# Performance work log

Hardware: AMD Instinct MI355X
Metric: run time of the kernel (lower is better)

## Reference

```python
import jax, jax.numpy as jnp
import numpy as np

B, D, C, OUT = 16384, 784, 2048, 10

def setup_inputs() -> dict:
    key = jax.random.key(0)
    k1, k2, k3 = jax.random.split(key, 3)
    x = jax.random.normal(k1, (B, D), dtype=jnp.float32)
    centres = jax.random.normal(k2, (C, D), dtype=jnp.float32)
    log_sigmas = jnp.zeros((C,), dtype=jnp.float32)
    W = jax.random.normal(k3, (OUT, C), dtype=jnp.float32) * (1.0 / np.sqrt(C))
    b = jnp.zeros((OUT,), dtype=jnp.float32)
    return {"x": x, "centres": centres, "log_sigmas": log_sigmas, "W": W, "b": b}

def reference(x, centres, log_sigmas, W, b):
    # (B, C, D) broadcast tensor the torch code materializes; same math).
    x2 = jnp.sum(x * x, axis=-1, keepdims=True)          # (B, 1)
    c2 = jnp.sum(centres * centres, axis=-1)             # (C,)
    d2 = jnp.maximum(x2 + c2[None, :] - 2.0 * (x @ centres.T), 0.0)  # (B, C)
    distances = jnp.sqrt(d2) / jnp.exp(log_sigmas)[None, :]          # (B, C)
    phi = jnp.exp(-(distances * distances))              # gaussian basis
    return phi @ W.T + b                                  # (B, OUT)
```

## Files before the change

kernel.cpp:

```cpp
#include <hip/hip_runtime.h>


#define B_ROWS 16384
#define D_DIM  784
#define C_DIM  2048
#define NOUT   10
#define KPAD   832
#define NKC    26
#define NCG    128
#define LOG2E  1.4426950408889634f

typedef __attribute__((ext_vector_type(8))) __bf16 bf16x8;
typedef __attribute__((ext_vector_type(4))) float  f32x4;
typedef __attribute__((ext_vector_type(4))) unsigned short ushort4v;

__device__ __forceinline__ unsigned short f2bf(float f) {
  union { float f; unsigned int u; } v; v.f = f;
  unsigned int u = v.u;
  return (unsigned short)((u + 0x7fffu + ((u >> 16) & 1u)) >> 16);
}

__device__ __forceinline__ void async16(const __bf16* g, __bf16* l) {
  __builtin_amdgcn_global_load_lds((const __attribute__((address_space(1))) void*)g,
                                   (__attribute__((address_space(3))) void*)l,
                                   16, 0, 0);
}

__global__ __launch_bounds__(256) void prep_rows(const float* __restrict__ src,
                                                 unsigned short* __restrict__ dst,
                                                 float* __restrict__ sq) {
  const int row  = blockIdx.x * 4 + (threadIdx.x >> 6);
  const int lane = threadIdx.x & 63;
  const float* s = src + (size_t)row * D_DIM;
  unsigned short* d = dst + (size_t)row * KPAD;
  float acc = 0.f;
#pragma unroll
  for (int c = 0; c < 4; ++c) {
    const int ch = lane + c * 64;
    if (ch < 196) {
      const float4 v = ((const float4*)s)[ch];
      ushort4v o; o.x = f2bf(v.x); o.y = f2bf(v.y); o.z = f2bf(v.z); o.w = f2bf(v.w);
      *(ushort4v*)(d + ch * 4) = o;
      acc += v.x * v.x + v.y * v.y + v.z * v.z + v.w * v.w;
    } else if (ch < 208) {
      ushort4v z = {0, 0, 0, 0};
      *(ushort4v*)(d + ch * 4) = z;
    }
  }
#pragma unroll
  for (int off = 32; off > 0; off >>= 1) acc += __shfl_down(acc, off);
  if (lane == 0) sq[row] = acc;
}

__global__ __launch_bounds__(256) void prep_cpack(const float* __restrict__ cen,
                                                  unsigned short* __restrict__ dst) {
  const int tile = blockIdx.x * 4 + (threadIdx.x >> 6);
  const int lane = threadIdx.x & 63;
  const int kc = tile >> 7;
  const int cg = tile & 127;
  const int c  = cg * 16 + (lane & 15);
  const int k  = kc * 32 + (lane >> 4) * 8;
  ushort4v o0 = {0, 0, 0, 0}, o1 = {0, 0, 0, 0};
  if (k + 8 <= D_DIM) {
    const float4 v0 = *(const float4*)(cen + (size_t)c * D_DIM + k);
    const float4 v1 = *(const float4*)(cen + (size_t)c * D_DIM + k + 4);
    o0.x = f2bf(v0.x); o0.y = f2bf(v0.y); o0.z = f2bf(v0.z); o0.w = f2bf(v0.w);
    o1.x = f2bf(v1.x); o1.y = f2bf(v1.y); o1.z = f2bf(v1.z); o1.w = f2bf(v1.w);
  }
  unsigned short* p = dst + ((size_t)tile * 64 + lane) * 8;
  *(ushort4v*)p = o0;
  *(ushort4v*)(p + 4) = o1;
}

__global__ __launch_bounds__(256) void prep_csq(const float* __restrict__ cen,
                                                float* __restrict__ sq) {
  const int row  = blockIdx.x * 4 + (threadIdx.x >> 6);
  const int lane = threadIdx.x & 63;
  const float* s = cen + (size_t)row * D_DIM;
  float acc = 0.f;
#pragma unroll
  for (int c = 0; c < 4; ++c) {
    const int ch = lane + c * 64;
    if (ch < 196) {
      const float4 v = ((const float4*)s)[ch];
      acc += v.x * v.x + v.y * v.y + v.z * v.z + v.w * v.w;
    }
  }
#pragma unroll
  for (int off = 32; off > 0; off >>= 1) acc += __shfl_down(acc, off);
  if (lane == 0) sq[row] = acc;
}

__global__ __launch_bounds__(256) void prep_misc(const float* __restrict__ ls,
                                                 const float* __restrict__ W,
                                                 const float* __restrict__ bias,
                                                 float* __restrict__ scale,
                                                 unsigned short* __restrict__ wb,
                                                 float* __restrict__ out) {
  const int i = blockIdx.x * 256 + threadIdx.x;
  if (i < B_ROWS * NOUT) out[i] = bias[i % NOUT];
  const int j = i - B_ROWS * NOUT;
  if (j >= 0 && j < 16 * C_DIM)
    wb[j] = ((j >> 11) < NOUT) ? f2bf(W[(j >> 11) * C_DIM + (j & 2047)]) : (unsigned short)0;
  const int k = j - 16 * C_DIM;
  if (k >= 0 && k < C_DIM) scale[k] = __expf(-2.f * ls[k]) * LOG2E;
}

__global__ __launch_bounds__(256, 4) void rbf_main(
    const __bf16* __restrict__ xb, const bf16x8* __restrict__ cbp,
    const __bf16* __restrict__ wb,
    const float* __restrict__ x2, const float* __restrict__ c2,
    const float* __restrict__ scale, float* __restrict__ out) {
  __shared__ char smem[34816];
  __bf16* As = (__bf16*)smem;
  __bf16* Ph = (__bf16*)smem;
  __shared__ float x2s[128], c2s[128], scs[128];

  const int tid  = threadIdx.x;
  const int w    = tid >> 6;
  const int lane = tid & 63;
  const int q    = lane >> 4;
  const int l16  = lane & 15;
  const int brow = blockIdx.x * 128;
  const int bcol = blockIdx.y * 128;

  if (tid < 128) x2s[tid] = x2[brow + tid];
  else { c2s[tid - 128] = c2[bcol + tid - 128]; scs[tid - 128] = scale[bcol + tid - 128]; }

  const int srow = tid >> 3;
  const int skc  = (tid & 7) ^ (srow & 7);
  const __bf16* gA = xb + (size_t)(brow + srow) * KPAD + skc * 8;
  __bf16* lA = As + w * 512;

  const int wr = (w >> 1) * 64;
  const int wc = (w & 1) * 64;
  const int cgb = (bcol >> 4) + (w & 1) * 4;
  const int swz = l16 & 7;

  f32x4 acc[4][4] = {};

#pragma unroll 1
  for (int it = 0; it < NKC / 2; ++it) {
    const int k0 = it * 64;
#pragma unroll
    for (int r = 0; r < 4; ++r)
      async16(gA + (size_t)r * 32 * KPAD + k0, lA + r * 2048);
    __syncthreads();
#pragma unroll
    for (int ks = 0; ks < 2; ++ks) {
      const int kc = it * 2 + ks;
      bf16x8 af[4], bfr[4];
#pragma unroll
      for (int j = 0; j < 4; ++j)
        bfr[j] = cbp[((size_t)kc * NCG + cgb + j) * 64 + lane];
#pragma unroll
      for (int i = 0; i < 4; ++i)
        af[i] = *(const bf16x8*)&As[(wr + i * 16 + l16) * 64 + (((ks * 4 + q) ^ swz) << 3)];
#pragma unroll
      for (int i = 0; i < 4; ++i)
#pragma unroll
        for (int j = 0; j < 4; ++j)
          acc[i][j] = __builtin_amdgcn_mfma_f32_16x16x32_bf16(af[i], bfr[j], acc[i][j], 0, 0, 0);
    }
    __syncthreads();
  }

#pragma unroll
  for (int i = 0; i < 4; ++i) {
    float xv[4];
#pragma unroll
    for (int r = 0; r < 4; ++r) xv[r] = x2s[wr + i * 16 + q * 4 + r];
#pragma unroll
    for (int j = 0; j < 4; ++j) {
      const int cl = wc + j * 16 + l16;
      const float c2v = c2s[cl];
      const float sc = scs[cl];
#pragma unroll
      for (int r = 0; r < 4; ++r) {
        const int rl = wr + i * 16 + q * 4 + r;
        const float d2 = fmaxf(fmaf(-2.f, acc[i][j][r], xv[r] + c2v), 0.f);
        Ph[rl * 136 + cl] = (__bf16)__builtin_exp2f(-d2 * sc);
      }
    }
  }
  __syncthreads();

  f32x4 oacc[2] = {};
#pragma unroll
  for (int kk = 0; kk < 4; ++kk) {
    const bf16x8 bw = *(const bf16x8*)&wb[(size_t)l16 * C_DIM + bcol + kk * 32 + q * 8];
#pragma unroll
    for (int mi = 0; mi < 2; ++mi) {
      const bf16x8 ap = *(const bf16x8*)&Ph[(w * 32 + mi * 16 + l16) * 136 + kk * 32 + q * 8];
      oacc[mi] = __builtin_amdgcn_mfma_f32_16x16x32_bf16(ap, bw, oacc[mi], 0, 0, 0);
    }
  }
  if (l16 < NOUT) {
#pragma unroll
    for (int mi = 0; mi < 2; ++mi)
#pragma unroll
      for (int r = 0; r < 4; ++r) {
        const int grow = brow + w * 32 + mi * 16 + q * 4 + r;
        atomicAdd(&out[grow * NOUT + l16], oacc[mi][r]);
      }
  }
}

extern "C" void kernel_launch(void* const* d_in, const int* in_sizes, int n_in,
                              void* d_out, int out_size, void* d_ws, size_t ws_size,
                              hipStream_t stream) {
  const float* x    = (const float*)d_in[0];
  const float* cen  = (const float*)d_in[1];
  const float* ls   = (const float*)d_in[2];
  const float* W    = (const float*)d_in[3];
  const float* bias = (const float*)d_in[4];
  float* out = (float*)d_out;

  unsigned char* ws = (unsigned char*)d_ws;
  unsigned short* xb  = (unsigned short*)(ws);
  unsigned short* cbp = (unsigned short*)(ws + 27262976);
  unsigned short* wb  = (unsigned short*)(ws + 30670848);
  float* x2 = (float*)(ws + 30736384);
  float* c2 = (float*)(ws + 30801920);
  float* sc = (float*)(ws + 30810112);

  prep_rows<<<B_ROWS / 4, 256, 0, stream>>>(x, xb, x2);
  prep_cpack<<<(NKC * NCG) / 4, 256, 0, stream>>>(cen, cbp);
  prep_csq<<<C_DIM / 4, 256, 0, stream>>>(cen, c2);
  prep_misc<<<(B_ROWS * NOUT + 16 * C_DIM + C_DIM + 255) / 256, 256, 0, stream>>>(
      ls, W, bias, sc, wb, out);
  rbf_main<<<dim3(B_ROWS / 128, C_DIM / 128), 256, 0, stream>>>(
      (const __bf16*)xb, (const bf16x8*)cbp, (const __bf16*)wb, x2, c2, sc, out);
}
```

Before: 170.7 us.

## Double-buffer A tiles in LDS and prefetch B fragments one K-step ahead

Restructures the main GEMM loop from a single-buffered 64-wide K step to a double-buffered 32-wide K step. The next A tile is loaded asynchronously into the alternate LDS buffer and the next centre fragments are loaded into registers while the current MFMAs run, so there is one barrier per iteration instead of two. This trades more iterations and more live registers for overlap of global load latency with compute.

Measured after the change: 170.1 us. Within noise of the previous version (-0.4%).

```diff
diff --git a/kernel.cpp b/kernel.cpp
--- a/kernel.cpp
+++ b/kernel.cpp
@@ -20,7 +20,7 @@
   return (unsigned short)((u + 0x7fffu + ((u >> 16) & 1u)) >> 16);
 }
 
-__device__ __forceinline__ void async16(const __bf16* g, __bf16* l) {
+__device__ __forceinline__ void async16(const __bf16* g, const __bf16* l) {
   __builtin_amdgcn_global_load_lds((const __attribute__((address_space(1))) void*)g,
                                    (__attribute__((address_space(3))) void*)l,
                                    16, 0, 0);
@@ -127,43 +127,49 @@
   if (tid < 128) x2s[tid] = x2[brow + tid];
   else { c2s[tid - 128] = c2[bcol + tid - 128]; scs[tid - 128] = scale[bcol + tid - 128]; }
 
-  const int srow = tid >> 3;
-  const int skc  = (tid & 7) ^ (srow & 7);
-  const __bf16* gA = xb + (size_t)(brow + srow) * KPAD + skc * 8;
-  __bf16* lA = As + w * 512;
+  const int srow = tid >> 2;
+  const int scg  = (tid & 3) ^ (srow & 3);
+  const __bf16* gA = xb + (size_t)(brow + srow) * KPAD + scg * 8;
+  const __bf16* lAw = As + w * 512;
 
   const int wr = (w >> 1) * 64;
   const int wc = (w & 1) * 64;
-  const int cgb = (bcol >> 4) + (w & 1) * 4;
-  const int swz = l16 & 7;
+  const bf16x8* cbw = cbp + ((size_t)((bcol >> 4) + (w & 1) * 4)) * 64 + lane;
 
   f32x4 acc[4][4] = {};
 
-#pragma unroll 1
-  for (int it = 0; it < NKC / 2; ++it) {
-    const int k0 = it * 64;
-#pragma unroll
-    for (int r = 0; r < 4; ++r)
-      async16(gA + (size_t)r * 32 * KPAD + k0, lA + r * 2048);
+#pragma unroll
+  for (int r = 0; r < 2; ++r)
+    async16(gA + (size_t)r * 64 * KPAD, lAw + r * 2048);
+  bf16x8 bcur[4], bnxt[4];
+#pragma unroll
+  for (int j = 0; j < 4; ++j) bcur[j] = cbw[j * 64];
+
+#pragma unroll 2
+  for (int it = 0; it < NKC; ++it) {
     __syncthreads();
-#pragma unroll
-    for (int ks = 0; ks < 2; ++ks) {
-      const int kc = it * 2 + ks;
-      bf16x8 af[4], bfr[4];
+    const int itn = (it + 1 < NKC) ? it + 1 : NKC - 1;
+    const __bf16* lAn = lAw + ((it + 1) & 1) * 4096;
+#pragma unroll
+    for (int r = 0; r < 2; ++r)
+      async16(gA + (size_t)r * 64 * KPAD + itn * 32, lAn + r * 2048);
+#pragma unroll
+    for (int j = 0; j < 4; ++j) bnxt[j] = cbw[((size_t)itn * NCG + j) * 64];
+
+    const __bf16* bufc = As + (it & 1) * 4096;
+    bf16x8 af[4];
+#pragma unroll
+    for (int i = 0; i < 4; ++i)
+      af[i] = *(const bf16x8*)&bufc[(wr + i * 16 + l16) * 32 + ((q ^ (l16 & 3)) << 3)];
+#pragma unroll
+    for (int i = 0; i < 4; ++i)
 #pragma unroll
       for (int j = 0; j < 4; ++j)
-        bfr[j] = cbp[((size_t)kc * NCG + cgb + j) * 64 + lane];
-#pragma unroll
-      for (int i = 0; i < 4; ++i)
-        af[i] = *(const bf16x8*)&As[(wr + i * 16 + l16) * 64 + (((ks * 4 + q) ^ swz) << 3)];
-#pragma unroll
-      for (int i = 0; i < 4; ++i)
-#pragma unroll
-        for (int j = 0; j < 4; ++j)
-          acc[i][j] = __builtin_amdgcn_mfma_f32_16x16x32_bf16(af[i], bfr[j], acc[i][j], 0, 0, 0);
-    }
-    __syncthreads();
-  }
+        acc[i][j] = __builtin_amdgcn_mfma_f32_16x16x32_bf16(af[i], bcur[j], acc[i][j], 0, 0, 0);
+#pragma unroll
+    for (int j = 0; j < 4; ++j) bcur[j] = bnxt[j];
+  }
+  __syncthreads();
 
 #pragma unroll
   for (int i = 0; i < 4; ++i) {
```
